# Optimization experiments

Measured on AMD Instinct MI355X. Metric: run time of the kernel, lower is better.

## Reference

```python
import jax, jax.numpy as jnp
import numpy as np

N_QUBITS = 12
Q_DEPTH = 3
N_GEN = 2
BATCH = 4096
TEMPERATURE = 5.0
DATA_REUPLOADING = False
DIM = 2 ** N_QUBITS


def setup_inputs() -> dict:
    key = jax.random.key(0)
    k1, k2, k3, k4 = jax.random.split(key, 4)
    x = jax.random.uniform(k1, (BATCH, N_QUBITS), jnp.float32) * (np.pi / 2)
    q_params = jax.random.uniform(k2, (N_GEN, Q_DEPTH * N_QUBITS * 3), jnp.float32)  # q_delta=1
    lin_w = jax.random.normal(k3, (DIM, N_QUBITS), jnp.float32) / np.sqrt(N_QUBITS)
    lin_b = jax.random.normal(k4, (DIM,), jnp.float32) * 0.01
    valid_state_mask = jnp.ones((DIM,), jnp.float32)
    return {"x": x, "q_params": q_params, "lin_w": lin_w, "lin_b": lin_b,
            "valid_state_mask": valid_state_mask}


def _ry(t):
    c, s = jnp.cos(t / 2), jnp.sin(t / 2)
    m = jnp.stack([jnp.stack([c, -s], -1), jnp.stack([s, c], -1)], -2)
    return m.astype(jnp.complex64)


def _rx(t):
    c = jnp.cos(t / 2).astype(jnp.complex64)
    s = (-1j) * jnp.sin(t / 2).astype(jnp.complex64)
    return jnp.stack([jnp.stack([c, s], -1), jnp.stack([s, c], -1)], -2)


def _rz(t):
    e = jnp.exp(-0.5j * t.astype(jnp.complex64))
    z = jnp.zeros_like(e)
    return jnp.stack([jnp.stack([e, z], -1), jnp.stack([z, jnp.conj(e)], -1)], -2)


def _apply_1q(state, U, wire):
    # state: (B, 2, 2, ..., 2); U: (2,2) shared or (B,2,2) per-sample
    ax = 1 + wire
    s = jnp.moveaxis(state, ax, -1)
    if U.ndim == 3:
        s = jnp.einsum('b...i,bji->b...j', s, U)
    else:
        s = jnp.einsum('...i,ji->...j', s, U)
    return jnp.moveaxis(s, -1, ax)


def _cnot(state, c, t):
    s = jnp.moveaxis(state, (1 + c, 1 + t), (1, 2))
    s = jnp.stack([s[:, 0], s[:, 1, ::-1]], axis=1)  # flip target where control=1
    return jnp.moveaxis(s, (1, 2), (1 + c, 1 + t))


def _circuit_probs(x, weights):
    # x: (B, n_qubits) noise; weights: (q_depth*n_qubits*3,)
    B = x.shape[0]
    state = jnp.zeros((B,) + (2,) * N_QUBITS, jnp.complex64)
    state = state.at[(slice(None),) + (0,) * N_QUBITS].set(1.0)
    w = weights.reshape(Q_DEPTH, N_QUBITS * 3)
    for i in range(Q_DEPTH):
        if DATA_REUPLOADING or i == 0:
            for j in range(N_QUBITS):
                state = _apply_1q(state, _ry(x[:, j]), j)
        for y in range(N_QUBITS):
            state = _apply_1q(state, _rz(w[i, 3 * y]), y)
            state = _apply_1q(state, _rx(w[i, 3 * y + 1]), y)
            state = _apply_1q(state, _ry(w[i, 3 * y + 2]), y)
        for y in range(N_QUBITS - 1):
            state = _cnot(state, y, y + 1)
        state = _cnot(state, N_QUBITS - 1, 0)  # python for-else always runs
    amp = state.reshape(B, DIM)
    return (amp.real ** 2 + amp.imag ** 2).astype(jnp.float32)


def reference(x, q_params, lin_w, lin_b, valid_state_mask):
    outputs = jnp.concatenate([_circuit_probs(x, q_params[g]) for g in range(N_GEN)], axis=1)
    converted_x = (x @ lin_w.T + lin_b) * TEMPERATURE
    return outputs, converted_x
```

## Files before the change

kernel.cpp:

```cpp
#include <hip/hip_runtime.h>

#define NQ     12
#define DIM    4096
#define BATCH  4096
#define NGEN   2

typedef float f32x2 __attribute__((ext_vector_type(2)));

constexpr unsigned cnot_map(unsigned b, int c, int t) {
  return b ^ (((b >> c) & 1u) << t);
}
constexpr unsigned ring_fwd(unsigned b) {
  b = cnot_map(b, 0, 11);
  for (int y = 10; y >= 0; --y) b = cnot_map(b, 11 - y, 10 - y);
  return b;
}
constexpr unsigned ring_inv(unsigned b) {
  for (int y = 0; y <= 10; ++y) b = cnot_map(b, 11 - y, 10 - y);
  b = cnot_map(b, 0, 11);
  return b;
}
constexpr unsigned pw (unsigned b, int k) { for (int r = 0; r < k; ++r) b = ring_fwd(b); return b; }
constexpr unsigned pwi(unsigned b, int k) { for (int r = 0; r < k; ++r) b = ring_inv(b); return b; }
constexpr int parity12(unsigned x) { int p = 0; for (int j = 0; j < 12; ++j) p ^= (x >> j) & 1; return p; }

struct QT {
  unsigned short v[2][12];
  unsigned short c[2][12];
};
constexpr QT make_qt() {
  QT t{};
  for (int li = 0; li < 2; ++li)
    for (int y = 0; y < 12; ++y) {
      const int p = 11 - y;
      t.v[li][y] = (unsigned short)pw(1u << p, li + 1);
      unsigned cm = 0;
      for (int j = 0; j < 12; ++j)
        cm |= (unsigned)((pwi(1u << j, li + 1) >> p) & 1u) << j;
      t.c[li][y] = (unsigned short)cm;
    }
  return t;
}
constexpr QT qt = make_qt();

constexpr bool ortho_ok() {
  for (int li = 0; li < 2; ++li)
    for (int a = 0; a < 12; ++a)
      for (int b = 0; b < 12; ++b)
        if (parity12((unsigned)qt.v[li][a] & (unsigned)qt.c[li][b]) != (a == b ? 1 : 0))
          return false;
  if (ring_inv(ring_fwd(0xABCu)) != 0xABCu) return false;
  return true;
}
static_assert(ortho_ok(), "GF(2) orthogonality violated");

constexpr unsigned A12(unsigned q) { return (q ^ (q >> 4) ^ (q >> 8)) & 0xFFFu; }

constexpr int msb12(unsigned x) { int m = -1; for (int i = 0; i < 12; ++i) if ((x >> i) & 1) m = i; return m; }
constexpr bool bins(unsigned* byMsb, unsigned x) {
  while (x) { int m = msb12(x); if (!byMsb[m]) { byMsb[m] = x; return true; } x ^= byMsb[m]; }
  return false;
}

struct GTab {
  unsigned lut[6][256];
  unsigned short gv[6][16];
  unsigned short sflo[256];
  unsigned short sfhi[16];
  unsigned char ok;
};
constexpr GTab make_gtab() {
  GTab t{};
  bool good = true;
  for (int li = 0; li < 2; ++li)
    for (int gi = 0; gi < 3; ++gi) {
      const int gid = li * 3 + gi;
      unsigned v[4], cm[4];
      for (int b = 0; b < 4; ++b) { v[b] = qt.v[li][gi * 4 + b]; cm[b] = qt.c[li][gi * 4 + b]; }
      unsigned byMsb[12] = {};
      for (int b = 0; b < 4; ++b) if (!bins(byMsb, v[b])) good = false;
      int Tpos[8] = {}; int c = 0;
      for (int cand = 0; cand < 12 && c < 8; ++cand)
        if (bins(byMsb, 1u << cand)) Tpos[c++] = cand;
      if (c != 8) good = false;
      for (int tid = 0; tid < 256; ++tid) {
        unsigned q = 0;
        for (int cc = 0; cc < 8; ++cc) if ((tid >> cc) & 1) q ^= 1u << Tpos[cc];
        unsigned pb = 0;
        for (int b = 0; b < 4; ++b) pb |= (unsigned)parity12(q & cm[b]) << b;
        t.lut[gid][tid] = (pb << 16) | (A12(q) << 3);
      }
      for (int j = 0; j < 16; ++j) {
        unsigned g = 0;
        for (int b = 0; b < 4; ++b) if ((j >> b) & 1) g ^= v[b];
        t.gv[gid][j] = (unsigned short)A12(g);
      }
      bool seen[4096] = {};
      for (int tid = 0; tid < 256; ++tid)
        for (int j = 0; j < 16; ++j) {
          unsigned idx = ((t.lut[gid][tid] & 0xFFFFu) >> 3) ^ (unsigned)t.gv[gid][j];
          if (idx >= 4096 || seen[idx]) good = false;
          seen[idx] = true;
        }
    }
  for (int tid = 0; tid < 256; ++tid) t.sflo[tid] = (unsigned short)A12(pw((unsigned)tid, 3));
  for (int k = 0; k < 16; ++k)       t.sfhi[k]   = (unsigned short)A12(pw((unsigned)k << 8, 3));
  t.ok = good ? 1 : 0;
  return t;
}
constexpr GTab h_gtab = make_gtab();
static_assert(h_gtab.ok == 1, "group tables inconsistent");
__constant__ GTab d_gtab = make_gtab();

__device__ __forceinline__ float2 cmuls(float2 a, float2 b) {
  return make_float2(a.x * b.x - a.y * b.y, a.x * b.y + a.y * b.x);
}
__device__ __forceinline__ float2 cadds(float2 a, float2 b) {
  return make_float2(a.x + b.x, a.y + b.y);
}
__device__ __forceinline__ void mat2mul(const float2* A, const float2* B, float2* C) {
  C[0] = cadds(cmuls(A[0], B[0]), cmuls(A[1], B[2]));
  C[1] = cadds(cmuls(A[0], B[1]), cmuls(A[1], B[3]));
  C[2] = cadds(cmuls(A[2], B[0]), cmuls(A[3], B[2]));
  C[3] = cadds(cmuls(A[2], B[1]), cmuls(A[3], B[3]));
}
__device__ __forceinline__ void fusedU(float a, float b, float c, float2* U) {
  float sa, ca, sb, cb, sc, cc;
  sincosf(a * 0.5f, &sa, &ca);
  sincosf(b * 0.5f, &sb, &cb);
  sincosf(c * 0.5f, &sc, &cc);
  float2 RZ[4] = { {ca, -sa}, {0.f, 0.f}, {0.f, 0.f}, {ca, sa} };
  float2 RX[4] = { {cb, 0.f}, {0.f, -sb}, {0.f, -sb}, {cb, 0.f} };
  float2 RY[4] = { {cc, 0.f}, {-sc, 0.f}, {sc, 0.f}, {cc, 0.f} };
  float2 M[4];
  mat2mul(RX, RZ, M);
  mat2mul(RY, M, U);
}

__device__ __forceinline__ f32x2 pcmul(f32x2 a, f32x2 b) {
  return (f32x2){a.x, a.x} * b + (f32x2){-a.y, a.y} * (f32x2){b.y, b.x};
}
__device__ __forceinline__ float xorf(float f, unsigned m) {
  return __uint_as_float(__float_as_uint(f) ^ m);
}

__device__ __forceinline__ f32x2 pk_mul_dl(f32x2 a, f32x2 b) {
  f32x2 d;
  asm("v_pk_mul_f32 %0, %1, %2 op_sel:[0,0] op_sel_hi:[0,1]" : "=v"(d) : "v"(a), "v"(b));
  return d;
}
__device__ __forceinline__ f32x2 pk_f1(f32x2 a, f32x2 s, f32x2 c) {
  f32x2 d;
  asm("v_pk_fma_f32 %0, %1, %2, %3 op_sel:[0,1,0] op_sel_hi:[0,0,1] neg_lo:[1,0,0]"
      : "=v"(d) : "v"(a), "v"(s), "v"(c));
  return d;
}
__device__ __forceinline__ f32x2 pk_f1b(f32x2 a, f32x2 s, f32x2 c) {
  f32x2 d;
  asm("v_pk_fma_f32 %0, %1, %2, %3 op_sel:[0,1,0] op_sel_hi:[0,0,1] neg_hi:[1,0,0]"
      : "=v"(d) : "v"(a), "v"(s), "v"(c));
  return d;
}
__device__ __forceinline__ f32x2 pk_f2(f32x2 a, f32x2 s, f32x2 c) {
  f32x2 d;
  asm("v_pk_fma_f32 %0, %1, %2, %3 op_sel:[1,0,0] op_sel_hi:[1,1,1]"
      : "=v"(d) : "v"(a), "v"(s), "v"(c));
  return d;
}
__device__ __forceinline__ f32x2 pk_f2b(f32x2 a, f32x2 s, f32x2 c) {
  f32x2 d;
  asm("v_pk_fma_f32 %0, %1, %2, %3 op_sel:[1,0,0] op_sel_hi:[1,1,1] neg_lo:[1,0,0] neg_hi:[1,0,0]"
      : "=v"(d) : "v"(a), "v"(s), "v"(c));
  return d;
}
__device__ __forceinline__ f32x2 pk_f3(f32x2 a, f32x2 s, f32x2 c) {
  f32x2 d;
  asm("v_pk_fma_f32 %0, %1, %2, %3 op_sel:[1,1,0] op_sel_hi:[1,0,1] neg_lo:[1,0,0]"
      : "=v"(d) : "v"(a), "v"(s), "v"(c));
  return d;
}

template<int GID>
__device__ __forceinline__ void do_pass(f32x2* st, const f32x2 (*gAB)[2], unsigned L) {
  const unsigned tbB = L & 0xFFFFu;
  const unsigned pb  = L >> 16;
  char* stb = (char*)st;

  f32x2 e[16];
  #pragma unroll
  for (int j = 0; j < 16; ++j)
    e[j] = *(const f32x2*)(stb + (tbB ^ ((unsigned)h_gtab.gv[GID][j] << 3)));

  constexpr int gbase = (GID / 3) * 12 + (GID % 3) * 4;
  #pragma unroll
  for (int b = 0; b < 4; ++b) {
    const f32x2 ga = gAB[gbase + b][0];
    const f32x2 gb = gAB[gbase + b][1];
    const unsigned sg = ((pb >> b) & 1u) << 31;
    f32x2 q;
    q.x = xorf(ga.y, sg);
    q.y = xorf(gb.x, sg);
    #pragma unroll
    for (int j0 = 0; j0 < 16; ++j0) {
      if (j0 & (1 << b)) continue;
      const int j1 = j0 | (1 << b);
      const f32x2 s0 = e[j0], s1 = e[j1];
      f32x2 t0 = pk_mul_dl(ga, s0);
      t0 = pk_f1(q, s0, t0);
      t0 = pk_f2(q, s1, t0);
      t0 = pk_f3(gb, s1, t0);
      f32x2 t1 = pk_mul_dl(ga, s1);
      t1 = pk_f1b(q, s1, t1);
      t1 = pk_f2b(q, s0, t1);
      t1 = pk_f3(gb, s0, t1);
      e[j0] = t0;
      e[j1] = t1;
    }
  }
  #pragma unroll
  for (int j = 0; j < 16; ++j)
    *(f32x2*)(stb + (tbB ^ ((unsigned)h_gtab.gv[GID][j] << 3))) = e[j];
}

__global__ __launch_bounds__(256, 4) void qcirc_kernel(const float* __restrict__ x,
                                                       const float* __restrict__ qp,
                                                       const float* __restrict__ lw,
                                                       const float* __restrict__ lb,
                                                       float* __restrict__ out) {
  __shared__ f32x2 st[DIM];
  __shared__ f32x2 gAB[24][2];
  __shared__ f32x2 vq[NQ][2];

  const int tid = threadIdx.x;
  const int s = blockIdx.x >> 1;
  const int g = blockIdx.x & 1;

  unsigned lutr[6];
  #pragma unroll
  for (int i = 0; i < 6; ++i) lutr[i] = d_gtab.lut[i][tid];
  const unsigned sflo = d_gtab.sflo[tid];
  float xr[NQ];
  #pragma unroll
  for (int jj = 0; jj < 3; ++jj)
    *(float4*)&xr[jj * 4] = *(const float4*)&x[s * NQ + jj * 4];

  if (tid < 24) {
    const int li = tid / 12, y = tid % 12;
    const float* w = qp + g * 108 + (li + 1) * 36 + 3 * y;
    float2 U[4];
    fusedU(w[0], w[1], w[2], U);
    gAB[tid][0] = (f32x2){U[0].x, U[0].y};
    gAB[tid][1] = (f32x2){U[1].x, U[1].y};
  } else if (tid >= 64 && tid < 64 + NQ) {
    const int j = tid - 64;
    const float* w = qp + g * 108 + 3 * j;
    float2 U0[4];
    fusedU(w[0], w[1], w[2], U0);
    float cx, sx;
    sincosf(x[s * NQ + j] * 0.5f, &sx, &cx);
    vq[j][0] = (f32x2){U0[0].x * cx + U0[1].x * sx, U0[0].y * cx + U0[1].y * sx};
    vq[j][1] = (f32x2){U0[2].x * cx + U0[3].x * sx, U0[2].y * cx + U0[3].y * sx};
  }
  __syncthreads();

  {
    const unsigned bt = (unsigned)tid ^ ((unsigned)tid >> 4);
    f32x2 low = vq[11][tid & 1];
    #pragma unroll
    for (int p = 1; p < 8; ++p) low = pcmul(low, vq[11 - p][(tid >> p) & 1]);
    #pragma unroll
    for (int r = 0; r < 16; ++r) {
      f32x2 h = vq[3][r & 1];
      h = pcmul(h, vq[2][(r >> 1) & 1]);
      h = pcmul(h, vq[1][(r >> 2) & 1]);
      h = pcmul(h, vq[0][(r >> 3) & 1]);
      st[(r * 0x111) ^ bt] = pcmul(low, h);
    }
  }

  __syncthreads(); do_pass<0>(st, gAB, lutr[0]);
  __syncthreads(); do_pass<1>(st, gAB, lutr[1]);
  __syncthreads(); do_pass<2>(st, gAB, lutr[2]);
  __syncthreads(); do_pass<3>(st, gAB, lutr[3]);
  __syncthreads(); do_pass<4>(st, gAB, lutr[4]);
  __syncthreads(); do_pass<5>(st, gAB, lutr[5]);
  __syncthreads();

  float* ob = out + (size_t)s * (NGEN * DIM) + (size_t)g * DIM;
  #pragma unroll
  for (int k = 0; k < 16; ++k) {
    const f32x2 a = st[(sflo ^ (unsigned)h_gtab.sfhi[k])];
    ob[k * 256 + tid] = a.x * a.x + a.y * a.y;
  }

  float* o2 = out + (size_t)BATCH * NGEN * DIM + (size_t)s * DIM;
  #pragma unroll
  for (int it = 0; it < 2; ++it) {
    const int d0 = g * 2048 + it * 1024 + tid * 4;
    const float4 b4 = *(const float4*)&lb[d0];
    float4 r;
    float* rp = &r.x;
    const float* bp = &b4.x;
    #pragma unroll
    for (int dd = 0; dd < 4; ++dd) {
      float acc = bp[dd];
      const float* wrow = lw + (size_t)(d0 + dd) * NQ;
      #pragma unroll
      for (int j = 0; j < NQ; ++j) acc = fmaf(xr[j], wrow[j], acc);
      rp[dd] = acc * 5.0f;
    }
    *(float4*)&o2[d0] = r;
  }
}

extern "C" void kernel_launch(void* const* d_in, const int* in_sizes, int n_in,
                              void* d_out, int out_size, void* d_ws, size_t ws_size,
                              hipStream_t stream) {
  const float* x    = (const float*)d_in[0];
  const float* qp   = (const float*)d_in[1];
  const float* linw = (const float*)d_in[2];
  const float* linb = (const float*)d_in[3];
  float* out = (float*)d_out;

  qcirc_kernel<<<BATCH * NGEN, 256, 0, stream>>>(x, qp, linw, linb, out);
}
```

Before: 353.2 us.

## Precompute gate matrices and initial qubit vectors in a separate prep kernel

Adds a small prep kernel that computes the fused layer gate coefficients and the per-sample first-layer product-state factors once and writes them to workspace. The main kernel then reads these from global memory instead of running sincos and matrix setup in shared memory with extra syncs in every block. It also raises the occupancy hint to 5 and builds the initial state with fewer complex multiplies. The cost is an extra launch and a global round-trip, and the path falls back to the old kernel when the workspace is too small.

```diff
diff --git a/kernel.cpp b/kernel.cpp
--- a/kernel.cpp
+++ b/kernel.cpp
@@ -112,6 +112,9 @@
 static_assert(h_gtab.ok == 1, "group tables inconsistent");
 __constant__ GTab d_gtab = make_gtab();
 
+#define WS_VQ_F4   64
+#define WS_NEEDED  (1024 + (size_t)BATCH * NGEN * NQ * 16)
+
 __device__ __forceinline__ float2 cmuls(float2 a, float2 b) {
   return make_float2(a.x * b.x - a.y * b.y, a.x * b.y + a.y * b.x);
 }
@@ -180,22 +183,11 @@
   return d;
 }
 
-template<int GID>
-__device__ __forceinline__ void do_pass(f32x2* st, const f32x2 (*gAB)[2], unsigned L) {
-  const unsigned tbB = L & 0xFFFFu;
-  const unsigned pb  = L >> 16;
-  char* stb = (char*)st;
-
-  f32x2 e[16];
-  #pragma unroll
-  for (int j = 0; j < 16; ++j)
-    e[j] = *(const f32x2*)(stb + (tbB ^ ((unsigned)h_gtab.gv[GID][j] << 3)));
-
-  constexpr int gbase = (GID / 3) * 12 + (GID % 3) * 4;
+__device__ __forceinline__ void bfly4(f32x2* e, const f32x2* ga4, const f32x2* gb4, unsigned pb) {
   #pragma unroll
   for (int b = 0; b < 4; ++b) {
-    const f32x2 ga = gAB[gbase + b][0];
-    const f32x2 gb = gAB[gbase + b][1];
+    const f32x2 ga = ga4[b];
+    const f32x2 gb = gb4[b];
     const unsigned sg = ((pb >> b) & 1u) << 31;
     f32x2 q;
     q.x = xorf(ga.y, sg);
@@ -217,9 +209,147 @@
       e[j1] = t1;
     }
   }
+}
+
+template<int GID>
+__device__ __forceinline__ void do_pass(f32x2* st, const float* __restrict__ gw, unsigned L) {
+  const unsigned tbB = L & 0xFFFFu;
+  const unsigned pb  = L >> 16;
+  char* stb = (char*)st;
+
+  f32x2 ga4[4], gb4[4];
+  #pragma unroll
+  for (int b = 0; b < 4; ++b) {
+    ga4[b] = (f32x2){gw[b * 4 + 0], gw[b * 4 + 1]};
+    gb4[b] = (f32x2){gw[b * 4 + 2], gw[b * 4 + 3]};
+  }
+
+  f32x2 e[16];
+  #pragma unroll
+  for (int j = 0; j < 16; ++j)
+    e[j] = *(const f32x2*)(stb + (tbB ^ ((unsigned)h_gtab.gv[GID][j] << 3)));
+
+  bfly4(e, ga4, gb4, pb);
+
   #pragma unroll
   for (int j = 0; j < 16; ++j)
     *(f32x2*)(stb + (tbB ^ ((unsigned)h_gtab.gv[GID][j] << 3))) = e[j];
+}
+
+__global__ __launch_bounds__(256) void prep_kernel(const float* __restrict__ x,
+                                                   const float* __restrict__ qp,
+                                                   float* __restrict__ ws) {
+  const int t = blockIdx.x * 256 + threadIdx.x;
+  if (t < 48) {
+    const int g = t / 24, k = t % 24;
+    const int li = k / 12, y = k % 12;
+    const float* w = qp + g * 108 + (li + 1) * 36 + 3 * y;
+    float2 U[4];
+    fusedU(w[0], w[1], w[2], U);
+    const int gid = li * 3 + y / 4, b = y % 4;
+    float* o = ws + (g * 6 + gid) * 16 + b * 4;
+    o[0] = U[0].x; o[1] = U[0].y; o[2] = U[1].x; o[3] = U[1].y;
+  }
+  const int s = t / 24, r = t % 24;
+  if (s < BATCH) {
+    const int g = r / 12, j = r % 12;
+    const float* w = qp + g * 108 + 3 * j;
+    float2 U0[4];
+    fusedU(w[0], w[1], w[2], U0);
+    float cx, sx;
+    sincosf(x[s * NQ + j] * 0.5f, &sx, &cx);
+    float4 o;
+    o.x = U0[0].x * cx + U0[1].x * sx;
+    o.y = U0[0].y * cx + U0[1].y * sx;
+    o.z = U0[2].x * cx + U0[3].x * sx;
+    o.w = U0[2].y * cx + U0[3].y * sx;
+    ((float4*)ws)[WS_VQ_F4 + s * 24 + r] = o;
+  }
+}
+
+__global__ __launch_bounds__(256, 5) void qcirc_fast(const float* __restrict__ x,
+                                                     const float* __restrict__ ws,
+                                                     const float* __restrict__ lw,
+                                                     const float* __restrict__ lb,
+                                                     float* __restrict__ out) {
+  __shared__ f32x2 st[DIM];
+
+  const int tid = threadIdx.x;
+  const int s = blockIdx.x >> 1;
+  const int g = blockIdx.x & 1;
+
+  unsigned lutr[6];
+  #pragma unroll
+  for (int i = 0; i < 6; ++i) lutr[i] = d_gtab.lut[i][tid];
+  const unsigned sflo = d_gtab.sflo[tid];
+
+  const float4* vqp = (const float4*)ws + WS_VQ_F4 + blockIdx.x * 12;
+  float4 vv[12];
+  #pragma unroll
+  for (int j = 0; j < 12; ++j) vv[j] = vqp[j];
+
+  {
+    const unsigned bt = (unsigned)tid ^ ((unsigned)tid >> 4);
+    f32x2 low = (tid & 1) ? (f32x2){vv[11].z, vv[11].w} : (f32x2){vv[11].x, vv[11].y};
+    #pragma unroll
+    for (int p = 1; p < 8; ++p) {
+      const float4 v = vv[11 - p];
+      const f32x2 f = ((tid >> p) & 1) ? (f32x2){v.z, v.w} : (f32x2){v.x, v.y};
+      low = pcmul(low, f);
+    }
+    f32x2 m0[4], m1[4];
+    #pragma unroll
+    for (int a = 0; a < 4; ++a) {
+      const f32x2 f3 = (a & 1) ? (f32x2){vv[3].z, vv[3].w} : (f32x2){vv[3].x, vv[3].y};
+      const f32x2 f2 = (a & 2) ? (f32x2){vv[2].z, vv[2].w} : (f32x2){vv[2].x, vv[2].y};
+      const f32x2 f1 = (a & 1) ? (f32x2){vv[1].z, vv[1].w} : (f32x2){vv[1].x, vv[1].y};
+      const f32x2 f0 = (a & 2) ? (f32x2){vv[0].z, vv[0].w} : (f32x2){vv[0].x, vv[0].y};
+      m0[a] = pcmul(f3, f2);
+      m1[a] = pcmul(f1, f0);
+    }
+    #pragma unroll
+    for (int r = 0; r < 16; ++r)
+      st[(r * 0x111) ^ bt] = pcmul(low, pcmul(m0[r & 3], m1[r >> 2]));
+  }
+
+  const float* gwb = ws + g * 96;
+  __syncthreads(); do_pass<0>(st, gwb +  0, lutr[0]);
+  __syncthreads(); do_pass<1>(st, gwb + 16, lutr[1]);
+  __syncthreads(); do_pass<2>(st, gwb + 32, lutr[2]);
+  __syncthreads(); do_pass<3>(st, gwb + 48, lutr[3]);
+  __syncthreads(); do_pass<4>(st, gwb + 64, lutr[4]);
+  __syncthreads(); do_pass<5>(st, gwb + 80, lutr[5]);
+  __syncthreads();
+
+  float* ob = out + (size_t)s * (NGEN * DIM) + (size_t)g * DIM;
+  #pragma unroll
+  for (int k = 0; k < 16; ++k) {
+    const f32x2 a = st[(sflo ^ (unsigned)h_gtab.sfhi[k])];
+    ob[k * 256 + tid] = a.x * a.x + a.y * a.y;
+  }
+
+  float xr[NQ];
+  #pragma unroll
+  for (int jj = 0; jj < 3; ++jj)
+    *(float4*)&xr[jj * 4] = *(const float4*)&x[s * NQ + jj * 4];
+  float* o2 = out + (size_t)BATCH * NGEN * DIM + (size_t)s * DIM;
+  #pragma unroll
+  for (int it = 0; it < 2; ++it) {
+    const int d0 = g * 2048 + it * 1024 + tid * 4;
+    const float4 b4 = *(const float4*)&lb[d0];
+    float4 r;
+    float* rp = &r.x;
+    const float* bp = &b4.x;
+    #pragma unroll
+    for (int dd = 0; dd < 4; ++dd) {
+      float acc = bp[dd];
+      const float* wrow = lw + (size_t)(d0 + dd) * NQ;
+      #pragma unroll
+      for (int j = 0; j < NQ; ++j) acc = fmaf(xr[j], wrow[j], acc);
+      rp[dd] = acc * 5.0f;
+    }
+    *(float4*)&o2[d0] = r;
+  }
 }
 
 __global__ __launch_bounds__(256, 4) void qcirc_kernel(const float* __restrict__ x,
@@ -278,12 +408,26 @@
     }
   }
 
-  __syncthreads(); do_pass<0>(st, gAB, lutr[0]);
-  __syncthreads(); do_pass<1>(st, gAB, lutr[1]);
-  __syncthreads(); do_pass<2>(st, gAB, lutr[2]);
-  __syncthreads(); do_pass<3>(st, gAB, lutr[3]);
-  __syncthreads(); do_pass<4>(st, gAB, lutr[4]);
-  __syncthreads(); do_pass<5>(st, gAB, lutr[5]);
+  #pragma unroll
+  for (int gid = 0; gid < 6; ++gid) {
+    __syncthreads();
+    const unsigned L   = lutr[gid];
+    const unsigned tbB = L & 0xFFFFu;
+    const unsigned pb  = L >> 16;
+    char* stb = (char*)st;
+    const int gbase = (gid / 3) * 12 + (gid % 3) * 4;
+    f32x2 ga4[4], gb4[4];
+    #pragma unroll
+    for (int b = 0; b < 4; ++b) { ga4[b] = gAB[gbase + b][0]; gb4[b] = gAB[gbase + b][1]; }
+    f32x2 e[16];
+    #pragma unroll
+    for (int j = 0; j < 16; ++j)
+      e[j] = *(const f32x2*)(stb + (tbB ^ ((unsigned)h_gtab.gv[gid][j] << 3)));
+    bfly4(e, ga4, gb4, pb);
+    #pragma unroll
+    for (int j = 0; j < 16; ++j)
+      *(f32x2*)(stb + (tbB ^ ((unsigned)h_gtab.gv[gid][j] << 3))) = e[j];
+  }
   __syncthreads();
 
   float* ob = out + (size_t)s * (NGEN * DIM) + (size_t)g * DIM;
@@ -322,5 +466,11 @@
   const float* linb = (const float*)d_in[3];
   float* out = (float*)d_out;
 
-  qcirc_kernel<<<BATCH * NGEN, 256, 0, stream>>>(x, qp, linw, linb, out);
-}
+  if (ws_size >= WS_NEEDED) {
+    float* ws = (float*)d_ws;
+    prep_kernel<<<(BATCH * 24 + 255) / 256, 256, 0, stream>>>(x, qp, ws);
+    qcirc_fast<<<BATCH * NGEN, 256, 0, stream>>>(x, ws, linw, linb, out);
+  } else {
+    qcirc_kernel<<<BATCH * NGEN, 256, 0, stream>>>(x, qp, linw, linb, out);
+  }
+}
```

After: 369.5 us. +4.6%, slower.
